# Kernel optimization log

Hardware: AMD Instinct MI355X
Metric: run time of the kernel (lower is better)

## Reference

```python
import jax, jax.numpy as jnp
import numpy as np
from jax.scipy.special import logsumexp

# Per-part vertex counts from the original module (vertexnum[1:])
VERTEXNUM = [45, 61, 43, 45, 92, 34, 41, 62, 44, 44, 58, 42, 40, 60, 41, 35, 64, 28, 50, 62]
OFFSETS = np.concatenate([[0], np.cumsum(VERTEXNUM)])  # 21 offsets, total 985
BATCH = 2048
TOTAL_V = int(OFFSETS[-1])  # 985

# geomloss SamplesLoss(loss='sinkhorn', p=2, blur=0.05):
#   cost C(x,y) = |x-y|^2 / 2, eps_final = blur^p = 0.0025,
#   eps-scaling annealing from ~diameter^2 down to blur^2 (scaling=0.5 -> x0.25 per step),
#   debiased divergence S = OT(x,y) - 0.5*OT(x,x) - 0.5*OT(y,y).
BLUR2 = 0.05 ** 2
DIAM2 = 64.0  # static diameter^2 estimate for unit-gaussian point clouds
_eps, EPS_LIST = DIAM2, []
while _eps > BLUR2:
    EPS_LIST.append(_eps)
    _eps *= 0.25
EPS_LIST.append(BLUR2)


def _sqdist(x, y):
    # x: [n,3], y: [m,3] -> 0.5*||x_i - y_j||^2, shape [n,m]
    x2 = jnp.sum(x * x, axis=-1)
    y2 = jnp.sum(y * y, axis=-1)
    return 0.5 * (x2[:, None] + y2[None, :] - 2.0 * (x @ y.T))


def _sinkhorn_div(x, y):
    # Debiased entropic OT (Sinkhorn divergence), uniform weights, symmetric log-domain updates.
    n, m = x.shape[0], y.shape[0]
    loga = -float(np.log(n))
    logb = -float(np.log(m))
    Cxy = _sqdist(x, y)
    Cxx = _sqdist(x, x)
    Cyy = _sqdist(y, y)
    f = jnp.zeros((n,), dtype=x.dtype)
    g = jnp.zeros((m,), dtype=x.dtype)
    px = jnp.zeros((n,), dtype=x.dtype)
    py = jnp.zeros((m,), dtype=x.dtype)
    for eps in EPS_LIST:
        ft = -eps * logsumexp((g[None, :] - Cxy) / eps + logb, axis=1)
        gt = -eps * logsumexp((f[:, None] - Cxy) / eps + loga, axis=0)
        f = 0.5 * (f + ft)
        g = 0.5 * (g + gt)
        px = 0.5 * (px - eps * logsumexp((px[None, :] - Cxx) / eps + loga, axis=1))
        py = 0.5 * (py - eps * logsumexp((py[None, :] - Cyy) / eps + logb, axis=1))
    # S = <a, f - px> + <b, g - py>  (uniform weights -> means)
    return jnp.mean(f - px) + jnp.mean(g - py)


def setup_inputs() -> dict:
    key = jax.random.key(0)
    k1, k2 = jax.random.split(key)
    predvert = jax.random.normal(k1, (BATCH, TOTAL_V, 3), dtype=jnp.float32)
    batch_pointclouds = jax.random.normal(k2, (BATCH, TOTAL_V, 3), dtype=jnp.float32)
    return {"predvert": predvert, "batch_pointclouds": batch_pointclouds}


def reference(predvert, batch_pointclouds):
    batch_size = predvert.shape[0]
    loss = jnp.asarray(0.0, dtype=predvert.dtype)
    for i in range(20):  # static loop over 20 structurally distinct parts
        s, e = int(OFFSETS[i]), int(OFFSETS[i + 1])
        xs = predvert[:, s:e, :]
        ys = batch_pointclouds[:, s:e, :]
        div = jax.vmap(_sinkhorn_div)(xs, ys)  # [B]
        loss = loss + jnp.sum(div) / batch_size
    return loss
```

## Files before the change

kernel.cpp:

```cpp
#include <hip/hip_runtime.h>
#include <math.h>

#define NPARTS 20
#define BATCH  2048
#define TOTALV 991
#define NEPS   9

#define LOG2E 1.4426950408889634f
#define LN2   0.6931471805599453f
#define NEGBIG -1.0e30f

__constant__ int   c_start[NPARTS] = {0,45,106,149,194,286,320,361,423,467,511,569,611,651,711,752,787,851,879,929};
__constant__ int   c_n[NPARTS]     = {45,61,43,45,92,34,41,62,44,44,58,42,40,60,41,35,64,28,50,62};
__constant__ float c_eps[NEPS]     = {64.0f,16.0f,4.0f,1.0f,0.25f,0.0625f,0.015625f,0.00390625f,0.0025f};

__constant__ int c_w_np[4]       = {4,5,5,6};
__constant__ int c_w_part[4][6]  = {{4,7,19,15,0,0},{16,1,13,12,17,0},{10,18,0,3,8,0},{9,2,11,6,14,5}};
__constant__ int c_w_lane0[4][7] = {{0,23,39,55,64,64,64},{0,16,32,47,57,64,64},{0,15,28,40,52,63,64},{0,11,22,33,44,55,64}};
__constant__ int c_w_tb[4][6]    = {{0,92,156,220,0,0},{0,64,128,188,228,0},{0,60,112,160,208,0},{0,44,88,132,176,220}};

#define NROWS 512

#define STREAM_UPDATE(A0,A1,A2, C0,C1A,C2A, TT, M, S) do { \
  const float w0_ = fmaf(A0, C0[0], fmaf(A1, C1A[0], fmaf(A2, C2A[0], TT[0]))); \
  const float w1_ = fmaf(A0, C0[1], fmaf(A1, C1A[1], fmaf(A2, C2A[1], TT[1]))); \
  const float w2_ = fmaf(A0, C0[2], fmaf(A1, C1A[2], fmaf(A2, C2A[2], TT[2]))); \
  const float w3_ = fmaf(A0, C0[3], fmaf(A1, C1A[3], fmaf(A2, C2A[3], TT[3]))); \
  const float mc_ = fmaxf(fmaxf(w0_, w1_), fmaxf(w2_, w3_)); \
  const float mn_ = fmaxf(M, mc_); \
  const float rr_ = __builtin_amdgcn_exp2f(M - mn_); \
  const float e0_ = __builtin_amdgcn_exp2f(w0_ - mn_); \
  const float e1_ = __builtin_amdgcn_exp2f(w1_ - mn_); \
  const float e2_ = __builtin_amdgcn_exp2f(w2_ - mn_); \
  const float e3_ = __builtin_amdgcn_exp2f(w3_ - mn_); \
  S = fmaf(S, rr_, (e0_ + e1_) + (e2_ + e3_)); \
  M = mn_; \
} while(0)

__global__ __launch_bounds__(128) void sinkhorn_kernel(
    const float* __restrict__ pred, const float* __restrict__ pc,
    float* __restrict__ partial)
{
    __shared__ float4 sC1[NROWS];
    __shared__ float2 sC2[NROWS];
    __shared__ float4 sS[NROWS];

    const int bid  = blockIdx.x;
    const int b    = bid >> 1;
    const int pair = bid & 1;
    const int wv   = threadIdx.x >> 6;
    const int lane = threadIdx.x & 63;
    const int w    = pair ? (wv ? 2 : 1) : (wv ? 3 : 0);
    const int rb   = wv << 8;

    int pj = -1;
    const int np = c_w_np[w];
    #pragma unroll
    for (int j = 0; j < 6; ++j)
        if (j < np && lane >= c_w_lane0[w][j] && lane < c_w_lane0[w][j+1]) pj = j;
    const bool lact = (pj >= 0);
    const int jj   = lact ? pj : 0;
    const int part = c_w_part[w][jj];
    const int st   = c_start[part];
    const int n    = lact ? c_n[part] : 0;
    const int h    = (n + 3) >> 2;
    const int r0   = lact ? (lane - c_w_lane0[w][jj]) : 0;
    const int tb   = rb + c_w_tb[w][jj];

    float x0r[4],x1r[4],x2r[4],y0r[4],y1r[4],y2r[4],xh[4],yh[4];
    bool ra[4];
    #pragma unroll
    for (int j=0;j<4;++j) {
        const int r = r0 + j*h;
        ra[j] = lact && (r < n);
        float a0=0.f,a1=0.f,a2=0.f,b0=0.f,b1=0.f,b2=0.f;
        if (ra[j]) {
            const float* xp = pred + ((size_t)b*TOTALV + st + r)*3;
            const float* yp = pc   + ((size_t)b*TOTALV + st + r)*3;
            a0=xp[0]; a1=xp[1]; a2=xp[2];
            b0=yp[0]; b1=yp[1]; b2=yp[2];
        }
        x0r[j]=a0; x1r[j]=a1; x2r[j]=a2;
        y0r[j]=b0; y1r[j]=b1; y2r[j]=b2;
        xh[j] = -0.5f*(a0*a0+a1*a1+a2*a2);
        yh[j] = -0.5f*(b0*b0+b1*b1+b2*b2);
    }
    #pragma unroll
    for (int j=0;j<4;++j) if (lact) {
        const int tr = tb + r0 + j*h;
        sC1[tr] = make_float4(x0r[j], x1r[j], x2r[j], y0r[j]);
        sC2[tr] = make_float2(y1r[j], y2r[j]);
    }

    const float lA = lact ? -log2f((float)n) : 0.f;
    float f[4]={0,0,0,0}, g[4]={0,0,0,0}, px[4]={0,0,0,0}, py[4]={0,0,0,0};

    #pragma unroll 1
    for (int it=0; it<NEPS; ++it) {
        const float eps = c_eps[it];
        const float sc  = LOG2E/eps;
        const float ce  = -eps*LN2;

        #pragma unroll
        for (int j=0;j<4;++j) if (lact) {
            const int tr = tb + r0 + j*h;
            if (ra[j])
                sS[tr] = make_float4(fmaf(sc, g[j]  + yh[j], lA),
                                     fmaf(sc, f[j]  + xh[j], lA),
                                     fmaf(sc, px[j] + xh[j], lA),
                                     fmaf(sc, py[j] + yh[j], lA));
            else
                sS[tr] = make_float4(NEGBIG, NEGBIG, NEGBIG, NEGBIG);
        }

        float mF[4],mG[4],mP[4],mQ[4],sF[4],sG[4],sP[4],sQ[4];
        #pragma unroll
        for (int j=0;j<4;++j) {
            mF[j]=-INFINITY; mG[j]=-INFINITY; mP[j]=-INFINITY; mQ[j]=-INFINITY;
            sF[j]=0.f; sG[j]=0.f; sP[j]=0.f; sQ[j]=0.f;
        }

        #pragma unroll 1
        for (int c=0; c<h; ++c) {
            const int row = tb + (c<<2);
            float cx0[4],cx1[4],cx2[4],cy0[4],cy1[4],cy2[4],tf[4],tg[4],tp[4],tq[4];
            #pragma unroll
            for (int kk=0;kk<4;++kk) {
                const float4 a = sC1[row+kk];
                const float2 c2 = sC2[row+kk];
                const float4 t = sS[row+kk];
                cx0[kk]=a.x*sc; cx1[kk]=a.y*sc; cx2[kk]=a.z*sc;
                cy0[kk]=a.w*sc; cy1[kk]=c2.x*sc; cy2[kk]=c2.y*sc;
                tf[kk]=t.x; tg[kk]=t.y; tp[kk]=t.z; tq[kk]=t.w;
            }
            #pragma unroll
            for (int j=0;j<4;++j) {
                STREAM_UPDATE(x0r[j],x1r[j],x2r[j], cy0,cy1,cy2, tf, mF[j], sF[j]);
                STREAM_UPDATE(y0r[j],y1r[j],y2r[j], cx0,cx1,cx2, tg, mG[j], sG[j]);
                STREAM_UPDATE(x0r[j],x1r[j],x2r[j], cx0,cx1,cx2, tp, mP[j], sP[j]);
                STREAM_UPDATE(y0r[j],y1r[j],y2r[j], cy0,cy1,cy2, tq, mQ[j], sQ[j]);
            }
        }

        if (lact) {
            #pragma unroll
            for (int j=0;j<4;++j) {
                const float ax = xh[j]*sc, ay = yh[j]*sc;
                f[j]  = 0.5f*(f[j]  + ce*(ax + mF[j] + __builtin_amdgcn_logf(sF[j])));
                g[j]  = 0.5f*(g[j]  + ce*(ay + mG[j] + __builtin_amdgcn_logf(sG[j])));
                px[j] = 0.5f*(px[j] + ce*(ax + mP[j] + __builtin_amdgcn_logf(sP[j])));
                py[j] = 0.5f*(py[j] + ce*(ay + mQ[j] + __builtin_amdgcn_logf(sQ[j])));
            }
        }
    }

    float d = 0.f;
    #pragma unroll
    for (int j=0;j<4;++j) if (ra[j]) d += (f[j]-px[j]) + (g[j]-py[j]);
    if (lact) d *= 1.0f/(float)n;
    #pragma unroll
    for (int o=32;o>0;o>>=1) d += __shfl_down(d, o, 64);
    if (lane==0) partial[(bid<<1)+wv] = d * (1.0f/(float)BATCH);
}

__global__ __launch_bounds__(1024) void reduce_kernel(
    const float* __restrict__ partial, float* __restrict__ out, int nb)
{
    const int t = threadIdx.x;
    double acc = 0.0;
    for (int i=t; i<nb; i+=blockDim.x) acc += (double)partial[i];
    #pragma unroll
    for (int o=32; o>0; o>>=1) acc += __shfl_down(acc, o, 64);
    __shared__ double ws[16];
    if ((t & 63) == 0) ws[t >> 6] = acc;
    __syncthreads();
    if (t == 0) {
        double tot = 0.0;
        for (int v=0; v<1024/64; ++v) tot += ws[v];
        out[0] = (float)tot;
    }
}

extern "C" void kernel_launch(void* const* d_in, const int* in_sizes, int n_in,
                              void* d_out, int out_size, void* d_ws, size_t ws_size,
                              hipStream_t stream) {
    const float* pred = (const float*)d_in[0];
    const float* pc   = (const float*)d_in[1];
    float* partial = (float*)d_ws;
    float* out     = (float*)d_out;
    sinkhorn_kernel<<<BATCH*2, 128, 0, stream>>>(pred, pc, partial);
    reduce_kernel<<<1, 1024, 0, stream>>>(partial, out, BATCH*4);
}
```

Baseline: 1.401 ms.

## Merge batch blocks, pre-scale coordinates in LDS, repack shared arrays

Each block now handles one batch element with four wavefronts, each taking a rotated part-group, in place of two blocks of two waves per batch. The shared-memory layout is repacked so coordinates are stored already multiplied by 1/eps and fused with the potentials, as sA/sB/sC. This removes six multiplies per streamed row in the inner loop, at the cost of rewriting the coordinates every eps step. The inner loop is also unrolled by two, and launch bounds of 256 threads with 3 blocks per CU may limit registers.

```diff
diff --git a/kernel.cpp b/kernel.cpp
--- a/kernel.cpp
+++ b/kernel.cpp
@@ -19,7 +19,7 @@
 __constant__ int c_w_lane0[4][7] = {{0,23,39,55,64,64,64},{0,16,32,47,57,64,64},{0,15,28,40,52,63,64},{0,11,22,33,44,55,64}};
 __constant__ int c_w_tb[4][6]    = {{0,92,156,220,0,0},{0,64,128,188,228,0},{0,60,112,160,208,0},{0,44,88,132,176,220}};
 
-#define NROWS 512
+#define NROWS 1024
 
 #define STREAM_UPDATE(A0,A1,A2, C0,C1A,C2A, TT, M, S) do { \
   const float w0_ = fmaf(A0, C0[0], fmaf(A1, C1A[0], fmaf(A2, C2A[0], TT[0]))); \
@@ -37,21 +37,19 @@
   M = mn_; \
 } while(0)
 
-__global__ __launch_bounds__(128) void sinkhorn_kernel(
+__global__ __launch_bounds__(256, 3) void sinkhorn_kernel(
     const float* __restrict__ pred, const float* __restrict__ pc,
     float* __restrict__ partial)
 {
-    __shared__ float4 sC1[NROWS];
-    __shared__ float2 sC2[NROWS];
-    __shared__ float4 sS[NROWS];
+    __shared__ float4 sA[NROWS];
+    __shared__ float4 sB[NROWS];
+    __shared__ float2 sC[NROWS];
 
-    const int bid  = blockIdx.x;
-    const int b    = bid >> 1;
-    const int pair = bid & 1;
+    const int b    = blockIdx.x;
     const int wv   = threadIdx.x >> 6;
     const int lane = threadIdx.x & 63;
-    const int w    = pair ? (wv ? 2 : 1) : (wv ? 3 : 0);
-    const int rb   = wv << 8;
+    const int w    = (wv + b) & 3;
+    const int rb   = w << 8;
 
     int pj = -1;
     const int np = c_w_np[w];
@@ -85,12 +83,6 @@
         xh[j] = -0.5f*(a0*a0+a1*a1+a2*a2);
         yh[j] = -0.5f*(b0*b0+b1*b1+b2*b2);
     }
-    #pragma unroll
-    for (int j=0;j<4;++j) if (lact) {
-        const int tr = tb + r0 + j*h;
-        sC1[tr] = make_float4(x0r[j], x1r[j], x2r[j], y0r[j]);
-        sC2[tr] = make_float2(y1r[j], y2r[j]);
-    }
 
     const float lA = lact ? -log2f((float)n) : 0.f;
     float f[4]={0,0,0,0}, g[4]={0,0,0,0}, px[4]={0,0,0,0}, py[4]={0,0,0,0};
@@ -104,13 +96,15 @@
         #pragma unroll
         for (int j=0;j<4;++j) if (lact) {
             const int tr = tb + r0 + j*h;
-            if (ra[j])
-                sS[tr] = make_float4(fmaf(sc, g[j]  + yh[j], lA),
-                                     fmaf(sc, f[j]  + xh[j], lA),
-                                     fmaf(sc, px[j] + xh[j], lA),
-                                     fmaf(sc, py[j] + yh[j], lA));
-            else
-                sS[tr] = make_float4(NEGBIG, NEGBIG, NEGBIG, NEGBIG);
+            if (ra[j]) {
+                sA[tr] = make_float4(y0r[j]*sc, y1r[j]*sc, y2r[j]*sc, fmaf(sc, g[j]  + yh[j], lA));
+                sB[tr] = make_float4(x0r[j]*sc, x1r[j]*sc, x2r[j]*sc, fmaf(sc, f[j]  + xh[j], lA));
+                sC[tr] = make_float2(fmaf(sc, py[j] + yh[j], lA), fmaf(sc, px[j] + xh[j], lA));
+            } else {
+                sA[tr] = make_float4(0.f, 0.f, 0.f, NEGBIG);
+                sB[tr] = make_float4(0.f, 0.f, 0.f, NEGBIG);
+                sC[tr] = make_float2(NEGBIG, NEGBIG);
+            }
         }
 
         float mF[4],mG[4],mP[4],mQ[4],sF[4],sG[4],sP[4],sQ[4];
@@ -120,18 +114,18 @@
             sF[j]=0.f; sG[j]=0.f; sP[j]=0.f; sQ[j]=0.f;
         }
 
-        #pragma unroll 1
+        #pragma unroll 2
         for (int c=0; c<h; ++c) {
             const int row = tb + (c<<2);
-            float cx0[4],cx1[4],cx2[4],cy0[4],cy1[4],cy2[4],tf[4],tg[4],tp[4],tq[4];
+            float cy0[4],cy1[4],cy2[4],cx0[4],cx1[4],cx2[4],tf[4],tg[4],tp[4],tq[4];
             #pragma unroll
             for (int kk=0;kk<4;++kk) {
-                const float4 a = sC1[row+kk];
-                const float2 c2 = sC2[row+kk];
-                const float4 t = sS[row+kk];
-                cx0[kk]=a.x*sc; cx1[kk]=a.y*sc; cx2[kk]=a.z*sc;
-                cy0[kk]=a.w*sc; cy1[kk]=c2.x*sc; cy2[kk]=c2.y*sc;
-                tf[kk]=t.x; tg[kk]=t.y; tp[kk]=t.z; tq[kk]=t.w;
+                const float4 a4 = sA[row+kk];
+                const float4 b4 = sB[row+kk];
+                const float2 c2 = sC[row+kk];
+                cy0[kk]=a4.x; cy1[kk]=a4.y; cy2[kk]=a4.z; tf[kk]=a4.w;
+                cx0[kk]=b4.x; cx1[kk]=b4.y; cx2[kk]=b4.z; tg[kk]=b4.w;
+                tq[kk]=c2.x; tp[kk]=c2.y;
             }
             #pragma unroll
             for (int j=0;j<4;++j) {
@@ -160,7 +154,7 @@
     if (lact) d *= 1.0f/(float)n;
     #pragma unroll
     for (int o=32;o>0;o>>=1) d += __shfl_down(d, o, 64);
-    if (lane==0) partial[(bid<<1)+wv] = d * (1.0f/(float)BATCH);
+    if (lane==0) partial[(b<<2)+wv] = d * (1.0f/(float)BATCH);
 }
 
 __global__ __launch_bounds__(1024) void reduce_kernel(
@@ -188,6 +182,6 @@
     const float* pc   = (const float*)d_in[1];
     float* partial = (float*)d_ws;
     float* out     = (float*)d_out;
-    sinkhorn_kernel<<<BATCH*2, 128, 0, stream>>>(pred, pc, partial);
+    sinkhorn_kernel<<<BATCH, 256, 0, stream>>>(pred, pc, partial);
     reduce_kernel<<<1, 1024, 0, stream>>>(partial, out, BATCH*4);
 }
```

Result: faster. 1.184 ms (-15.4%).
